# Optimization experiments

Measured on AMD Instinct MI355X. Metric: run time of the kernel, lower is better.

## Reference

```python
import jax, jax.numpy as jnp
import numpy as np

N, E = 50000, 800000
NODE_IN, EDGE_IN, HID, OUT = 64, 16, 64, 32
BN_EPS = 1e-5


def _linear_params(key, fan_in, fan_out):
    kw, kb = jax.random.split(key)
    lim = 1.0 / np.sqrt(fan_in)
    W = jax.random.uniform(kw, (fan_in, fan_out), minval=-lim, maxval=lim, dtype=jnp.float32)
    b = jax.random.uniform(kb, (fan_out,), minval=-lim, maxval=lim, dtype=jnp.float32)
    return W, b


def setup_inputs() -> dict:
    key = jax.random.key(0)
    ks = jax.random.split(key, 8)
    x = jax.random.normal(ks[0], (N, NODE_IN), dtype=jnp.float32)
    edge_index = jax.random.randint(ks[1], (2, E), 0, N, dtype=jnp.int64)
    edge_attr = jax.random.normal(ks[2], (E, EDGE_IN), dtype=jnp.float32)
    # layer 1: message Linear(node_in + edge_in -> hid), self Linear(node_in -> hid)
    W1_msg, b1_msg = _linear_params(ks[3], NODE_IN + EDGE_IN, HID)
    W1_self, b1_self = _linear_params(ks[4], NODE_IN, HID)
    # BatchNorm1d(hidden) params (inference mode: running stats)
    bn_gamma = jnp.ones((HID,), jnp.float32)
    bn_beta = jnp.zeros((HID,), jnp.float32)
    bn_mean = jax.random.normal(ks[5], (HID,), dtype=jnp.float32) * 0.1
    bn_var = jax.random.uniform(ks[6], (HID,), minval=0.5, maxval=1.5, dtype=jnp.float32)
    # layer 2: message Linear(hid + edge_in -> out), self Linear(hid -> out)
    k7, k8 = jax.random.split(ks[7])
    W2_msg, b2_msg = _linear_params(k7, HID + EDGE_IN, OUT)
    W2_self, b2_self = _linear_params(k8, HID, OUT)
    return dict(x=x, edge_index=edge_index, edge_attr=edge_attr,
                W1_msg=W1_msg, b1_msg=b1_msg, W1_self=W1_self, b1_self=b1_self,
                bn_gamma=bn_gamma, bn_beta=bn_beta, bn_mean=bn_mean, bn_var=bn_var,
                W2_msg=W2_msg, b2_msg=b2_msg, W2_self=W2_self, b2_self=b2_self)


def _gnn_layer(x, edge_index, edge_attr, W_msg, b_msg, W_self, b_self):
    # gather source node features per edge, concat edge features, linear, scatter-sum to dst
    src, dst = edge_index[0], edge_index[1]
    m = jnp.concatenate([x[src], edge_attr], axis=-1) @ W_msg + b_msg  # [E, out]
    agg = jax.ops.segment_sum(m, dst, num_segments=x.shape[0])          # [N, out]
    return x @ W_self + b_self + agg


def reference(x, edge_index, edge_attr,
              W1_msg, b1_msg, W1_self, b1_self,
              bn_gamma, bn_beta, bn_mean, bn_var,
              W2_msg, b2_msg, W2_self, b2_self):
    h = _gnn_layer(x, edge_index, edge_attr, W1_msg, b1_msg, W1_self, b1_self)
    # BatchNorm1d (eval mode, running stats) + ReLU; dropout is identity in eval
    h = (h - bn_mean) * jax.lax.rsqrt(bn_var + BN_EPS) * bn_gamma + bn_beta
    h = jax.nn.relu(h)
    return _gnn_layer(h, edge_index, edge_attr, W2_msg, b2_msg, W2_self, b2_self)
```

## Files before the change

kernel.cpp:

```cpp
#include <hip/hip_runtime.h>

#define NN 50000
#define NE 800000
#define NB 6250
#define NT 3125
#define NBK 128
#define BNODE 391
#define BCAP 7680
#define SCAP 56
#define BINBLK 256
#define PREPBLK 64

typedef __attribute__((ext_vector_type(8))) short short8x;
typedef __attribute__((ext_vector_type(4))) float f32x4;

#define OFF_CNT   0LL
#define OFF_ROW   ((long long)NN)
#define OFF_RECS  (3LL*NN + 16)
#define OFF_FLAGS (35LL*NN + 16)
#define OFF_PK    (35LL*NN + 256)
#define OFF_FB1S  (35LL*NN + 7936)
#define OFF_FB2S  (35LL*NN + 8000)
#define OFF_F1    (36LL*NN)
#define OFF_F2    (116LL*NN)
#define OFF_Y2B   (164LL*NN)
#define OFF_BCUR  (212LL*NN)

__device__ __forceinline__ float ldf(const void* p, long long i, int bf16) {
  if (bf16) {
    unsigned short u = ((const unsigned short*)p)[i];
    return __uint_as_float(((unsigned)u) << 16);
  }
  return ((const float*)p)[i];
}
__device__ __forceinline__ unsigned short f2bf(float f) {
  unsigned u = __float_as_uint(f);
  unsigned r = (u + 0x7fffu + ((u >> 16) & 1u)) >> 16;
  return (unsigned short)r;
}
__device__ __forceinline__ unsigned pk2(float lo, float hi) {
  return (unsigned)f2bf(lo) | ((unsigned)f2bf(hi) << 16);
}
__device__ __forceinline__ int ldidx(const void* p, long long i, int i64) {
  return i64 ? (int)((const long long*)p)[i] : ((const int*)p)[i];
}
__device__ __forceinline__ float bflo(unsigned u) { return __uint_as_float(u << 16); }
__device__ __forceinline__ float bfhi(unsigned u) { return __uint_as_float(u & 0xffff0000u); }

__global__ __launch_bounds__(256) void k_prepbin(
    const void* __restrict__ ei, const void* __restrict__ x,
    const void* __restrict__ W1_msg, const void* __restrict__ b1_msg,
    const void* __restrict__ W1_self, const void* __restrict__ b1_self,
    const void* __restrict__ gamma, const void* __restrict__ beta,
    const void* __restrict__ mean, const void* __restrict__ var,
    const void* __restrict__ W2_msg, const void* __restrict__ b2_msg,
    const void* __restrict__ W2_self, const void* __restrict__ b2_self,
    int* __restrict__ flags, unsigned short* __restrict__ PK,
    float* __restrict__ fb1s, float* __restrict__ fb2s,
    int* __restrict__ bcur, int2* __restrict__ binbuf) {
  int tid = threadIdx.x;
  int lane = tid & 63;
  if (blockIdx.x < BINBLK) {
    __shared__ int2 stage[NBK][SCAP];
    __shared__ int scnt[NBK];
    __shared__ int gbase[NBK];
    __shared__ int s_i64;
    for (int i = tid; i < NBK; i += 256) scnt[i] = 0;
    if (tid < 64) {
      const int* p = (const int*)ei;
      int any = 0;
      for (int i = lane; i < 256; i += 64) any |= p[2 * i + 1];
      unsigned long long anyb = __ballot(any != 0);
      if (lane == 0) s_i64 = (anyb == 0ull) ? 1 : 0;
    }
    __syncthreads();
    int i64 = s_i64;
    for (long long e0 = (long long)blockIdx.x * 256; e0 < NE;
         e0 += (long long)BINBLK * 256) {
      long long e = e0 + tid;
      if (e < NE) {
        int src = ldidx(ei, e, i64);
        int dst = ldidx(ei, NE + e, i64);
        int b = dst / BNODE;
        int dl = dst - b * BNODE;
        int2 ent = make_int2(src | (dl << 16), (int)e);
        int pos = atomicAdd(&scnt[b], 1);
        if (pos < SCAP) {
          stage[b][pos] = ent;
        } else {
          int gp = atomicAdd(&bcur[b], 1);
          binbuf[(long long)b * BCAP + gp] = ent;
        }
      }
    }
    __syncthreads();
    if (tid < NBK) {
      int cb = scnt[tid] < SCAP ? scnt[tid] : SCAP;
      gbase[tid] = atomicAdd(&bcur[tid], cb);
    }
    __syncthreads();
    int wv = tid >> 6, ln = tid & 63;
    for (int b = wv; b < NBK; b += 4) {
      int cb = scnt[b] < SCAP ? scnt[b] : SCAP;
      int gb = gbase[b];
      for (int i = ln; i < cb; i += 64)
        binbuf[(long long)b * BCAP + gb + i] = stage[b][i];
    }
  } else {
    __shared__ int s_bf;
    if (tid < 64) {
      const unsigned short* q = (const unsigned short*)x;
      int cntc = 0;
      for (int i = lane; i < 256; i += 64) {
        unsigned short w = q[2 * i];
        int e = (w >> 7) & 0xff;
        if (w == 0 || (e >= 110 && e <= 140)) cntc++;
      }
      for (int m = 1; m < 64; m <<= 1) cntc += __shfl_xor(cntc, m, 64);
      int bfv = (cntc >= 192) ? 1 : 0;
      if (blockIdx.x == BINBLK) {
        const int* p = (const int*)ei;
        int any = 0;
        for (int i = lane; i < 256; i += 64) any |= p[2 * i + 1];
        unsigned long long anyb = __ballot(any != 0);
        if (lane == 0) {
          flags[0] = (anyb == 0ull) ? 1 : 0;
          flags[1] = bfv;
        }
      }
      if (lane == 0) s_bf = bfv;
    }
    __syncthreads();
    int bf = s_bf;
    int t0 = (blockIdx.x - BINBLK) * 256 + tid;
    int stride = PREPBLK * 256;
    for (int i = t0; i < 10240; i += stride) {
      int j = i & 7, L = (i >> 3) & 63, t = (i >> 9) & 3, c = i >> 11;
      int k = c * 32 + ((L >> 4) << 3) + j;
      int col = t * 16 + (L & 15);
      float sc = ldf(gamma, col, bf) * rsqrtf(ldf(var, col, bf) + 1e-5f);
      float v;
      if (k < 64) v = ldf(W1_msg, k * 64 + col, bf) * sc;
      else if (k < 128) v = ldf(W1_self, (k - 64) * 64 + col, bf) * sc;
      else if (k < 144) v = ldf(W1_msg, (64 + k - 128) * 64 + col, bf) * sc;
      else if (k == 144) v = ldf(b1_msg, col, bf) * sc;
      else v = 0.0f;
      PK[i] = f2bf(v);
    }
    for (int i = t0; i < 2048; i += stride) {
      int j = i & 7, L = (i >> 3) & 63, t = (i >> 9) & 1, c = i >> 10;
      int k = c * 32 + ((L >> 4) << 3) + j;
      int col = t * 16 + (L & 15);
      PK[10240 + i] = f2bf(ldf(W2_msg, k * 32 + col, bf));
    }
    for (int i = t0; i < 3072; i += stride) {
      int j = i & 7, L = (i >> 3) & 63, t = (i >> 9) & 1, c = i >> 10;
      int k = c * 32 + ((L >> 4) << 3) + j;
      int col = t * 16 + (L & 15);
      float v;
      if (k < 64) v = ldf(W2_self, k * 32 + col, bf);
      else if (k < 80) v = ldf(W2_msg, k * 32 + col, bf);
      else if (k == 80) v = ldf(b2_msg, col, bf);
      else v = 0.0f;
      PK[12288 + i] = f2bf(v);
    }
    for (int i = t0; i < 64; i += stride) {
      float sc = ldf(gamma, i, bf) * rsqrtf(ldf(var, i, bf) + 1e-5f);
      fb1s[i] = ldf(b1_self, i, bf) * sc + ldf(beta, i, bf) - ldf(mean, i, bf) * sc;
    }
    for (int i = t0; i < 32; i += stride) fb2s[i] = ldf(b2_self, i, bf);
  }
}

__global__ __launch_bounds__(1024) void k_place(const int* __restrict__ bcur,
                                                const int2* __restrict__ binbuf,
                                                int* __restrict__ row_ptr,
                                                int2* __restrict__ recs) {
  __shared__ int2 outb[BCAP];
  __shared__ int lh[BNODE];
  __shared__ int lexc[BNODE];
  __shared__ int lcur[BNODE];
  __shared__ int sb[NBK];
  __shared__ int s_rbase;
  int b = blockIdx.x;
  int tid = threadIdx.x;
  int base = b * BNODE;
  int nn = NN - base < BNODE ? NN - base : BNODE;
  if (tid < NBK) sb[tid] = bcur[tid];
  for (int i = tid; i < BNODE; i += 1024) lh[i] = 0;
  __syncthreads();
  if (tid < 64) {
    int v = (tid < b ? sb[tid] : 0) + (tid + 64 < b ? sb[tid + 64] : 0);
    for (int off = 32; off > 0; off >>= 1) v += __shfl_down(v, off, 64);
    if (tid == 0) s_rbase = v;
  }
  int cnt = sb[b];
  __syncthreads();
  int rbase = s_rbase;
  for (int i = tid; i < cnt; i += 1024) {
    int dl = (binbuf[(long long)b * BCAP + i].x >> 16) & 0x3FF;
    atomicAdd(&lh[dl], 1);
  }
  __syncthreads();
  if (tid < 64) {
    int carry = 0;
    for (int c0 = 0; c0 < BNODE; c0 += 64) {
      int i = c0 + tid;
      int orig = (i < nn) ? lh[i] : 0;
      int v = orig;
      for (int off = 1; off < 64; off <<= 1) {
        int u = __shfl_up(v, off, 64);
        if (tid >= off) v += u;
      }
      if (i < nn) lexc[i] = carry + v - orig;
      carry += __shfl(v, 63, 64);
    }
  }
  __syncthreads();
  for (int i = tid; i < nn; i += 1024) {
    int e = lexc[i];
    row_ptr[base + i] = rbase + e;
    lcur[i] = e;
  }
  if (b == NBK - 1 && tid == 0) row_ptr[NN] = rbase + cnt;
  __syncthreads();
  for (int i = tid; i < cnt; i += 1024) {
    int2 ent = binbuf[(long long)b * BCAP + i];
    int dl = (ent.x >> 16) & 0x3FF;
    int p = atomicAdd(&lcur[dl], 1);
    outb[p] = make_int2(ent.x & 0xFFFF, ent.y);
  }
  __syncthreads();
  for (int i = tid; i < cnt; i += 1024) recs[rbase + i] = outb[i];
}

__global__ __launch_bounds__(256) void k_gather1(
    const void* __restrict__ x, const void* __restrict__ ea,
    const int* __restrict__ row_ptr, const int2* __restrict__ recs,
    const int* __restrict__ flags, unsigned short* __restrict__ F1,
    unsigned short* __restrict__ F2) {
  int lane = threadIdx.x & 63;
  int g = lane >> 3, c = lane & 7;
  int bf = flags[1];
  long long wid = ((long long)blockIdx.x * blockDim.x + threadIdx.x) >> 6;
  long long nw = ((long long)gridDim.x * blockDim.x) >> 6;
  for (long long b = wid; b < NB; b += nw) {
    int n = (int)(b * 8 + g);
    int beg = row_ptr[n];
    int deg = row_ptr[n + 1] - beg;
    float a0 = 0.f, a1 = 0.f, a2 = 0.f, a3 = 0.f, a4 = 0.f, a5 = 0.f, a6 = 0.f, a7 = 0.f;
    float e0 = 0.f, e1 = 0.f, e2 = 0.f, e3 = 0.f;
    uint4 xw;
    if (bf) {
      const unsigned short* xs = (const unsigned short*)x;
      const unsigned short* es = (const unsigned short*)ea;
      int t = 0;
      for (; t + 4 <= deg; t += 4) {
        int2 r0 = recs[beg + t + 0];
        int2 r1 = recs[beg + t + 1];
        int2 r2 = recs[beg + t + 2];
        int2 r3 = recs[beg + t + 3];
        uint4 w0 = *((const uint4*)(xs + ((long long)r0.x << 6)) + c);
        uint4 w1 = *((const uint4*)(xs + ((long long)r1.x << 6)) + c);
        uint4 w2 = *((const uint4*)(xs + ((long long)r2.x << 6)) + c);
        uint4 w3 = *((const uint4*)(xs + ((long long)r3.x << 6)) + c);
        a0 += bflo(w0.x) + bflo(w1.x) + bflo(w2.x) + bflo(w3.x);
        a1 += bfhi(w0.x) + bfhi(w1.x) + bfhi(w2.x) + bfhi(w3.x);
        a2 += bflo(w0.y) + bflo(w1.y) + bflo(w2.y) + bflo(w3.y);
        a3 += bfhi(w0.y) + bfhi(w1.y) + bfhi(w2.y) + bfhi(w3.y);
        a4 += bflo(w0.z) + bflo(w1.z) + bflo(w2.z) + bflo(w3.z);
        a5 += bfhi(w0.z) + bfhi(w1.z) + bfhi(w2.z) + bfhi(w3.z);
        a6 += bflo(w0.w) + bflo(w1.w) + bflo(w2.w) + bflo(w3.w);
        a7 += bfhi(w0.w) + bfhi(w1.w) + bfhi(w2.w) + bfhi(w3.w);
        if (c < 4) {
          uint2 q0 = *((const uint2*)(es + ((long long)r0.y << 4)) + c);
          uint2 q1 = *((const uint2*)(es + ((long long)r1.y << 4)) + c);
          uint2 q2 = *((const uint2*)(es + ((long long)r2.y << 4)) + c);
          uint2 q3 = *((const uint2*)(es + ((long long)r3.y << 4)) + c);
          e0 += bflo(q0.x) + bflo(q1.x) + bflo(q2.x) + bflo(q3.x);
          e1 += bfhi(q0.x) + bfhi(q1.x) + bfhi(q2.x) + bfhi(q3.x);
          e2 += bflo(q0.y) + bflo(q1.y) + bflo(q2.y) + bflo(q3.y);
          e3 += bfhi(q0.y) + bfhi(q1.y) + bfhi(q2.y) + bfhi(q3.y);
        }
      }
      for (; t < deg; ++t) {
        int2 r = recs[beg + t];
        uint4 w = *((const uint4*)(xs + ((long long)r.x << 6)) + c);
        a0 += bflo(w.x); a1 += bfhi(w.x);
        a2 += bflo(w.y); a3 += bfhi(w.y);
        a4 += bflo(w.z); a5 += bfhi(w.z);
        a6 += bflo(w.w); a7 += bfhi(w.w);
        if (c < 4) {
          uint2 q = *((const uint2*)(es + ((long long)r.y << 4)) + c);
          e0 += bflo(q.x); e1 += bfhi(q.x);
          e2 += bflo(q.y); e3 += bfhi(q.y);
        }
      }
      xw = *((const uint4*)(xs + ((long long)n << 6)) + c);
    } else {
      const float* xf = (const float*)x;
      const float* ef = (const float*)ea;
      for (int t = 0; t < deg; ++t) {
        int2 r = recs[beg + t];
        float4 w0 = *((const float4*)(xf + ((long long)r.x << 6)) + c * 2);
        float4 w1 = *((const float4*)(xf + ((long long)r.x << 6)) + c * 2 + 1);
        a0 += w0.x; a1 += w0.y; a2 += w0.z; a3 += w0.w;
        a4 += w1.x; a5 += w1.y; a6 += w1.z; a7 += w1.w;
        if (c < 4) {
          float4 q = *((const float4*)(ef + ((long long)r.y << 4)) + c);
          e0 += q.x; e1 += q.y; e2 += q.z; e3 += q.w;
        }
      }
      float4 p0 = *((const float4*)(xf + ((long long)n << 6)) + c * 2);
      float4 p1 = *((const float4*)(xf + ((long long)n << 6)) + c * 2 + 1);
      xw = make_uint4(pk2(p0.x, p0.y), pk2(p0.z, p0.w), pk2(p1.x, p1.y), pk2(p1.z, p1.w));
    }
    unsigned short* f1 = F1 + (long long)n * 160;
    unsigned short* f2 = F2 + (long long)n * 96;
    *((uint4*)f1 + c) = make_uint4(pk2(a0, a1), pk2(a2, a3), pk2(a4, a5), pk2(a6, a7));
    *((uint4*)(f1 + 64) + c) = xw;
    if (c < 4) {
      uint2 sp = make_uint2(pk2(e0, e1), pk2(e2, e3));
      *((uint2*)(f1 + 128) + c) = sp;
      *((uint2*)(f2 + 64) + c) = sp;
    }
    if (c == 4) {
      unsigned d = (unsigned)f2bf((float)deg);
      *((uint4*)(f1 + 144)) = make_uint4(d, 0u, 0u, 0u);
      *((uint4*)(f2 + 80)) = make_uint4(d, 0u, 0u, 0u);
    }
    if (c == 5) {
      *((uint4*)(f1 + 152)) = make_uint4(0u, 0u, 0u, 0u);
      *((uint4*)(f2 + 88)) = make_uint4(0u, 0u, 0u, 0u);
    }
  }
}

__global__ __launch_bounds__(256) void k_gemm1(
    const unsigned short* __restrict__ F1, const unsigned short* __restrict__ PK,
    const float* __restrict__ fb1s, unsigned short* __restrict__ F2,
    unsigned short* __restrict__ Y2B) {
  __shared__ unsigned short hsh[4][16 * 72];
  int lane = threadIdx.x & 63;
  int wv = threadIdx.x >> 6;
  int m = lane & 15, quad = lane >> 4;
  unsigned short* hs = hsh[wv];
  short8x Bf[20];
#pragma unroll
  for (int s = 0; s < 20; ++s) Bf[s] = *(const short8x*)(PK + (s * 64 + lane) * 8);
  short8x By[4];
#pragma unroll
  for (int s = 0; s < 4; ++s) By[s] = *(const short8x*)(PK + 10240 + (s * 64 + lane) * 8);
  long long gw = (long long)blockIdx.x * 4 + wv;
  long long nw = (long long)gridDim.x * 4;
  for (long long tile = gw; tile < NT; tile += nw) {
    long long n0 = tile * 16;
    const unsigned short* f1 = F1 + (n0 + m) * 160 + quad * 8;
    short8x A[5];
#pragma unroll
    for (int cc = 0; cc < 5; ++cc) A[cc] = *(const short8x*)(f1 + cc * 32);
    f32x4 acc[4];
#pragma unroll
    for (int t = 0; t < 4; ++t) {
      float b = fb1s[t * 16 + m];
      acc[t] = (f32x4){b, b, b, b};
    }
#pragma unroll
    for (int cc = 0; cc < 5; ++cc) {
#pragma unroll
      for (int t = 0; t < 4; ++t)
        acc[t] = __builtin_amdgcn_mfma_f32_16x16x32_bf16(A[cc], Bf[cc * 4 + t], acc[t], 0, 0, 0);
    }
#pragma unroll
    for (int t = 0; t < 4; ++t) {
#pragma unroll
      for (int i = 0; i < 4; ++i) {
        float h = fmaxf(acc[t][i], 0.0f);
        unsigned short us = f2bf(h);
        F2[(n0 + quad * 4 + i) * 96 + t * 16 + m] = us;
        hs[(quad * 4 + i) * 72 + t * 16 + m] = us;
      }
    }
    __builtin_amdgcn_sched_barrier(0);
    f32x4 yacc[2];
    yacc[0] = (f32x4){0.f, 0.f, 0.f, 0.f};
    yacc[1] = (f32x4){0.f, 0.f, 0.f, 0.f};
#pragma unroll
    for (int cc = 0; cc < 2; ++cc) {
      short8x Ah = *(const short8x*)(hs + m * 72 + cc * 32 + quad * 8);
#pragma unroll
      for (int t = 0; t < 2; ++t)
        yacc[t] = __builtin_amdgcn_mfma_f32_16x16x32_bf16(Ah, By[cc * 2 + t], yacc[t], 0, 0, 0);
    }
#pragma unroll
    for (int t = 0; t < 2; ++t) {
#pragma unroll
      for (int i = 0; i < 4; ++i)
        Y2B[(n0 + quad * 4 + i) * 32 + t * 16 + m] = f2bf(yacc[t][i]);
    }
    __builtin_amdgcn_sched_barrier(0);
  }
}

__global__ __launch_bounds__(256) void k_gg2(
    const unsigned short* __restrict__ F2, const unsigned short* __restrict__ PK,
    const float* __restrict__ fb2s, const unsigned short* __restrict__ Y2B,
    const int* __restrict__ row_ptr, const int2* __restrict__ recs,
    const int* __restrict__ flags, void* __restrict__ out) {
  __shared__ float sums[2][16][33];
  int tid = threadIdx.x;
  int lane = tid & 63;
  int wv = tid >> 6;
  int tp = wv >> 1;
  int th = wv & 1;
  long long tile = (long long)blockIdx.x * 2 + tp;
  int valid = tile < NT;
  if (valid) {
    int g = lane >> 3, c = lane & 7;
    int n = (int)(tile * 16 + th * 8 + g);
    int beg = row_ptr[n];
    int deg = row_ptr[n + 1] - beg;
    float s0 = 0.f, s1 = 0.f, s2 = 0.f, s3 = 0.f;
    int t = 0;
    for (; t + 4 <= deg; t += 4) {
      int2 r0 = recs[beg + t + 0];
      int2 r1 = recs[beg + t + 1];
      int2 r2 = recs[beg + t + 2];
      int2 r3 = recs[beg + t + 3];
      uint2 q0 = *((const uint2*)(Y2B + (long long)r0.x * 32) + c);
      uint2 q1 = *((const uint2*)(Y2B + (long long)r1.x * 32) + c);
      uint2 q2 = *((const uint2*)(Y2B + (long long)r2.x * 32) + c);
      uint2 q3 = *((const uint2*)(Y2B + (long long)r3.x * 32) + c);
      s0 += bflo(q0.x) + bflo(q1.x) + bflo(q2.x) + bflo(q3.x);
      s1 += bfhi(q0.x) + bfhi(q1.x) + bfhi(q2.x) + bfhi(q3.x);
      s2 += bflo(q0.y) + bflo(q1.y) + bflo(q2.y) + bflo(q3.y);
      s3 += bfhi(q0.y) + bfhi(q1.y) + bfhi(q2.y) + bfhi(q3.y);
    }
    for (; t < deg; ++t) {
      int2 r = recs[beg + t];
      uint2 q = *((const uint2*)(Y2B + (long long)r.x * 32) + c);
      s0 += bflo(q.x); s1 += bfhi(q.x);
      s2 += bflo(q.y); s3 += bfhi(q.y);
    }
    float* sr = &sums[tp][th * 8 + g][c * 4];
    sr[0] = s0; sr[1] = s1; sr[2] = s2; sr[3] = s3;
  }
  __syncthreads();
  if (valid) {
    int m = lane & 15, quad = lane >> 4;
    int bf = flags[1];
    long long n0 = tile * 16;
    const unsigned short* f2 = F2 + (n0 + m) * 96 + quad * 8;
    short8x A[3];
#pragma unroll
    for (int cc = 0; cc < 3; ++cc) A[cc] = *(const short8x*)(f2 + cc * 32);
    short8x Bf[3];
#pragma unroll
    for (int cc = 0; cc < 3; ++cc)
      Bf[cc] = *(const short8x*)(PK + 12288 + ((cc * 2 + th) * 64 + lane) * 8);
    f32x4 acc;
    float fb = fb2s[th * 16 + m];
#pragma unroll
    for (int i = 0; i < 4; ++i) acc[i] = fb + sums[tp][quad * 4 + i][th * 16 + m];
#pragma unroll
    for (int cc = 0; cc < 3; ++cc)
      acc = __builtin_amdgcn_mfma_f32_16x16x32_bf16(A[cc], Bf[cc], acc, 0, 0, 0);
#pragma unroll
    for (int i = 0; i < 4; ++i) {
      long long idx = (n0 + quad * 4 + i) * 32 + th * 16 + m;
      if (bf) ((unsigned short*)out)[idx] = f2bf(acc[i]);
      else ((float*)out)[idx] = acc[i];
    }
  }
}

extern "C" void kernel_launch(void* const* d_in, const int* in_sizes, int n_in,
                              void* d_out, int out_size, void* d_ws, size_t ws_size,
                              hipStream_t stream) {
  const void* x = d_in[0];
  const void* ei = d_in[1];
  const void* ea = d_in[2];
  const void* W1_msg = d_in[3];
  const void* b1_msg = d_in[4];
  const void* W1_self = d_in[5];
  const void* b1_self = d_in[6];
  const void* gamma = d_in[7];
  const void* beta = d_in[8];
  const void* mean = d_in[9];
  const void* var = d_in[10];
  const void* W2_msg = d_in[11];
  const void* b2_msg = d_in[12];
  const void* W2_self = d_in[13];
  const void* b2_self = d_in[14];

  float* ws = (float*)d_ws;
  int* row_ptr = (int*)(ws + OFF_ROW);
  int2* recs = (int2*)(ws + OFF_RECS);
  int* flags = (int*)(ws + OFF_FLAGS);
  unsigned short* PK = (unsigned short*)(ws + OFF_PK);
  float* fb1s = ws + OFF_FB1S;
  float* fb2s = ws + OFF_FB2S;
  unsigned short* F1 = (unsigned short*)(ws + OFF_F1);
  int2* binbuf = (int2*)(ws + OFF_F1);
  unsigned short* F2 = (unsigned short*)(ws + OFF_F2);
  unsigned short* Y2B = (unsigned short*)(ws + OFF_Y2B);
  int* bcur = (int*)(ws + OFF_BCUR);

  hipMemsetAsync(bcur, 0, NBK * sizeof(int), stream);
  hipLaunchKernelGGL(k_prepbin, dim3(BINBLK + PREPBLK), dim3(256), 0, stream, ei, x,
                     W1_msg, b1_msg, W1_self, b1_self, gamma, beta, mean, var, W2_msg,
                     b2_msg, W2_self, b2_self, flags, PK, fb1s, fb2s, bcur, binbuf);
  hipLaunchKernelGGL(k_place, dim3(NBK), dim3(1024), 0, stream, bcur, binbuf, row_ptr,
                     recs);

  int gblocks = (NB + 3) / 4;
  hipLaunchKernelGGL(k_gather1, dim3(gblocks), dim3(256), 0, stream, x, ea, row_ptr,
                     recs, flags, F1, F2);
  int mblocks = (NT + 3) / 4;
  hipLaunchKernelGGL(k_gemm1, dim3(mblocks), dim3(256), 0, stream, F1, PK, fb1s, F2,
                     Y2B);
  hipLaunchKernelGGL(k_gg2, dim3((NT + 1) / 2), dim3(256), 0, stream, F2, PK, fb2s,
                     Y2B, row_ptr, recs, flags, d_out);
}
```

Measured before the change: 212.3 us.

## Fuse layer-1 gather and GEMM into one kernel via LDS staging

Merges the gather kernel and the layer-1 MFMA GEMM kernel into a single kernel. Each block handles two 16-node tiles, stages the aggregated features in shared memory instead of writing and re-reading the global F1 buffer, and splits the output columns across two waves per tile. This removes one kernel launch and the F1 global round-trip. In exchange, each block now reloads the weight fragments per tile instead of keeping them in registers across a persistent loop, and adds block-wide barriers.

```diff
diff --git a/kernel.cpp b/kernel.cpp
--- a/kernel.cpp
+++ b/kernel.cpp
@@ -2,7 +2,6 @@
 
 #define NN 50000
 #define NE 800000
-#define NB 6250
 #define NT 3125
 #define NBK 128
 #define BNODE 391
@@ -14,7 +13,6 @@
 typedef __attribute__((ext_vector_type(8))) short short8x;
 typedef __attribute__((ext_vector_type(4))) float f32x4;
 
-#define OFF_CNT   0LL
 #define OFF_ROW   ((long long)NN)
 #define OFF_RECS  (3LL*NN + 16)
 #define OFF_FLAGS (35LL*NN + 16)
@@ -234,18 +232,25 @@
   for (int i = tid; i < cnt; i += 1024) recs[rbase + i] = outb[i];
 }
 
-__global__ __launch_bounds__(256) void k_gather1(
+__global__ __launch_bounds__(256) void k_gg1(
     const void* __restrict__ x, const void* __restrict__ ea,
     const int* __restrict__ row_ptr, const int2* __restrict__ recs,
-    const int* __restrict__ flags, unsigned short* __restrict__ F1,
-    unsigned short* __restrict__ F2) {
-  int lane = threadIdx.x & 63;
-  int g = lane >> 3, c = lane & 7;
+    const int* __restrict__ flags, const unsigned short* __restrict__ PK,
+    const float* __restrict__ fb1s, unsigned short* __restrict__ F2,
+    unsigned short* __restrict__ Y2B) {
+  __shared__ __align__(16) unsigned short fs[2][16][168];
+  __shared__ __align__(16) unsigned short hsh[2][16 * 72];
+  int tid = threadIdx.x;
+  int lane = tid & 63;
+  int wv = tid >> 6;
+  int tp = wv >> 1, th = wv & 1;
+  long long tile = (long long)blockIdx.x * 2 + tp;
+  int valid = tile < NT;
   int bf = flags[1];
-  long long wid = ((long long)blockIdx.x * blockDim.x + threadIdx.x) >> 6;
-  long long nw = ((long long)gridDim.x * blockDim.x) >> 6;
-  for (long long b = wid; b < NB; b += nw) {
-    int n = (int)(b * 8 + g);
+  int m = lane & 15, quad = lane >> 4;
+  if (valid) {
+    int g = lane >> 3, c = lane & 7;
+    int n = (int)(tile * 16 + th * 8 + g);
     int beg = row_ptr[n];
     int deg = row_ptr[n + 1] - beg;
     float a0 = 0.f, a1 = 0.f, a2 = 0.f, a3 = 0.f, a4 = 0.f, a5 = 0.f, a6 = 0.f, a7 = 0.f;
@@ -315,7 +320,7 @@
       float4 p1 = *((const float4*)(xf + ((long long)n << 6)) + c * 2 + 1);
       xw = make_uint4(pk2(p0.x, p0.y), pk2(p0.z, p0.w), pk2(p1.x, p1.y), pk2(p1.z, p1.w));
     }
-    unsigned short* f1 = F1 + (long long)n * 160;
+    unsigned short* f1 = &fs[tp][th * 8 + g][0];
     unsigned short* f2 = F2 + (long long)n * 96;
     *((uint4*)f1 + c) = make_uint4(pk2(a0, a1), pk2(a2, a3), pk2(a4, a5), pk2(a6, a7));
     *((uint4*)(f1 + 64) + c) = xw;
@@ -334,71 +339,56 @@
       *((uint4*)(f2 + 88)) = make_uint4(0u, 0u, 0u, 0u);
     }
   }
-}
-
-__global__ __launch_bounds__(256) void k_gemm1(
-    const unsigned short* __restrict__ F1, const unsigned short* __restrict__ PK,
-    const float* __restrict__ fb1s, unsigned short* __restrict__ F2,
-    unsigned short* __restrict__ Y2B) {
-  __shared__ unsigned short hsh[4][16 * 72];
-  int lane = threadIdx.x & 63;
-  int wv = threadIdx.x >> 6;
-  int m = lane & 15, quad = lane >> 4;
-  unsigned short* hs = hsh[wv];
-  short8x Bf[20];
-#pragma unroll
-  for (int s = 0; s < 20; ++s) Bf[s] = *(const short8x*)(PK + (s * 64 + lane) * 8);
-  short8x By[4];
-#pragma unroll
-  for (int s = 0; s < 4; ++s) By[s] = *(const short8x*)(PK + 10240 + (s * 64 + lane) * 8);
-  long long gw = (long long)blockIdx.x * 4 + wv;
-  long long nw = (long long)gridDim.x * 4;
-  for (long long tile = gw; tile < NT; tile += nw) {
+  __syncthreads();
+  if (valid) {
     long long n0 = tile * 16;
-    const unsigned short* f1 = F1 + (n0 + m) * 160 + quad * 8;
+    const unsigned short* f1 = &fs[tp][m][quad * 8];
     short8x A[5];
 #pragma unroll
     for (int cc = 0; cc < 5; ++cc) A[cc] = *(const short8x*)(f1 + cc * 32);
-    f32x4 acc[4];
-#pragma unroll
-    for (int t = 0; t < 4; ++t) {
-      float b = fb1s[t * 16 + m];
-      acc[t] = (f32x4){b, b, b, b};
-    }
-#pragma unroll
-    for (int cc = 0; cc < 5; ++cc) {
-#pragma unroll
-      for (int t = 0; t < 4; ++t)
-        acc[t] = __builtin_amdgcn_mfma_f32_16x16x32_bf16(A[cc], Bf[cc * 4 + t], acc[t], 0, 0, 0);
-    }
-#pragma unroll
-    for (int t = 0; t < 4; ++t) {
+    short8x Bf[10];
+#pragma unroll
+    for (int cc = 0; cc < 5; ++cc)
+#pragma unroll
+      for (int j = 0; j < 2; ++j)
+        Bf[cc * 2 + j] = *(const short8x*)(PK + ((cc * 4 + th * 2 + j) * 64 + lane) * 8);
+    f32x4 acc[2];
+#pragma unroll
+    for (int j = 0; j < 2; ++j) {
+      float b = fb1s[(th * 2 + j) * 16 + m];
+      acc[j] = (f32x4){b, b, b, b};
+    }
+#pragma unroll
+    for (int cc = 0; cc < 5; ++cc)
+#pragma unroll
+      for (int j = 0; j < 2; ++j)
+        acc[j] = __builtin_amdgcn_mfma_f32_16x16x32_bf16(A[cc], Bf[cc * 2 + j], acc[j], 0, 0, 0);
+    unsigned short* hs = hsh[tp];
+#pragma unroll
+    for (int j = 0; j < 2; ++j) {
 #pragma unroll
       for (int i = 0; i < 4; ++i) {
-        float h = fmaxf(acc[t][i], 0.0f);
+        float h = fmaxf(acc[j][i], 0.0f);
         unsigned short us = f2bf(h);
-        F2[(n0 + quad * 4 + i) * 96 + t * 16 + m] = us;
-        hs[(quad * 4 + i) * 72 + t * 16 + m] = us;
-      }
-    }
-    __builtin_amdgcn_sched_barrier(0);
-    f32x4 yacc[2];
-    yacc[0] = (f32x4){0.f, 0.f, 0.f, 0.f};
-    yacc[1] = (f32x4){0.f, 0.f, 0.f, 0.f};
+        F2[(n0 + quad * 4 + i) * 96 + (th * 2 + j) * 16 + m] = us;
+        hs[(quad * 4 + i) * 72 + (th * 2 + j) * 16 + m] = us;
+      }
+    }
+  }
+  __syncthreads();
+  if (valid) {
+    long long n0 = tile * 16;
+    const unsigned short* hs = hsh[tp];
+    f32x4 yacc = (f32x4){0.f, 0.f, 0.f, 0.f};
 #pragma unroll
     for (int cc = 0; cc < 2; ++cc) {
       short8x Ah = *(const short8x*)(hs + m * 72 + cc * 32 + quad * 8);
-#pragma unroll
-      for (int t = 0; t < 2; ++t)
-        yacc[t] = __builtin_amdgcn_mfma_f32_16x16x32_bf16(Ah, By[cc * 2 + t], yacc[t], 0, 0, 0);
-    }
-#pragma unroll
-    for (int t = 0; t < 2; ++t) {
-#pragma unroll
-      for (int i = 0; i < 4; ++i)
-        Y2B[(n0 + quad * 4 + i) * 32 + t * 16 + m] = f2bf(yacc[t][i]);
-    }
-    __builtin_amdgcn_sched_barrier(0);
+      short8x By = *(const short8x*)(PK + 10240 + ((cc * 2 + th) * 64 + lane) * 8);
+      yacc = __builtin_amdgcn_mfma_f32_16x16x32_bf16(Ah, By, yacc, 0, 0, 0);
+    }
+#pragma unroll
+    for (int i = 0; i < 4; ++i)
+      Y2B[(n0 + quad * 4 + i) * 32 + th * 16 + m] = f2bf(yacc[i]);
   }
 }
 
@@ -500,7 +490,6 @@
   unsigned short* PK = (unsigned short*)(ws + OFF_PK);
   float* fb1s = ws + OFF_FB1S;
   float* fb2s = ws + OFF_FB2S;
-  unsigned short* F1 = (unsigned short*)(ws + OFF_F1);
   int2* binbuf = (int2*)(ws + OFF_F1);
   unsigned short* F2 = (unsigned short*)(ws + OFF_F2);
   unsigned short* Y2B = (unsigned short*)(ws + OFF_Y2B);
@@ -513,12 +502,9 @@
   hipLaunchKernelGGL(k_place, dim3(NBK), dim3(1024), 0, stream, bcur, binbuf, row_ptr,
                      recs);
 
-  int gblocks = (NB + 3) / 4;
-  hipLaunchKernelGGL(k_gather1, dim3(gblocks), dim3(256), 0, stream, x, ea, row_ptr,
-                     recs, flags, F1, F2);
-  int mblocks = (NT + 3) / 4;
-  hipLaunchKernelGGL(k_gemm1, dim3(mblocks), dim3(256), 0, stream, F1, PK, fb1s, F2,
-                     Y2B);
-  hipLaunchKernelGGL(k_gg2, dim3((NT + 1) / 2), dim3(256), 0, stream, F2, PK, fb2s,
-                     Y2B, row_ptr, recs, flags, d_out);
-}
+  int fblocks = (NT + 1) / 2;
+  hipLaunchKernelGGL(k_gg1, dim3(fblocks), dim3(256), 0, stream, x, ea, row_ptr, recs,
+                     flags, PK, fb1s, F2, Y2B);
+  hipLaunchKernelGGL(k_gg2, dim3(fblocks), dim3(256), 0, stream, F2, PK, fb2s, Y2B,
+                     row_ptr, recs, flags, d_out);
+}
```

Result: faster. 207.0 us (-2.5%).
